# Kernel optimization log

Hardware: AMD Instinct MI355X
Metric: run time of the kernel (lower is better)

The kernel has to match this reference:

```python
import jax, jax.numpy as jnp
import numpy as np

EPS = 1e-5  # torch LayerNorm default

def setup_inputs() -> dict:
    key = jax.random.key(0)
    ks = jax.random.split(key, 4)
    S, B, D, BN = 4096, 8, 1024, 128
    x = jax.random.normal(ks[0], (S, B, D), dtype=jnp.float32)
    residual = jax.random.normal(ks[1], (B, S, D), dtype=jnp.float32)
    # xavier_uniform init for adapter projections
    lim_d = float(np.sqrt(6.0 / (D + BN)))
    W_down = jax.random.uniform(ks[2], (BN, D), minval=-lim_d, maxval=lim_d, dtype=jnp.float32)
    W_up = jax.random.uniform(ks[3], (D, BN), minval=-lim_d, maxval=lim_d, dtype=jnp.float32)
    return {
        "x": x,
        "residual": residual,
        "ln_gamma": jnp.ones((D,), jnp.float32),
        "ln_beta": jnp.zeros((D,), jnp.float32),
        "W_down": W_down,
        "b_down": jnp.zeros((BN,), jnp.float32),
        "W_up": W_up,
        "b_up": jnp.zeros((D,), jnp.float32),
    }

def reference(x, residual, ln_gamma, ln_beta, W_down, b_down, W_up, b_up):
    # ffn_fn is an opaque callable (treated as identity here); x: [S,B,D]
    x = x + jnp.swapaxes(residual, 0, 1)           # residual.transpose(0,1)
    shortcut = x
    # NaiveAdapter: LayerNorm -> down -> ReLU -> up -> residual add
    mu = jnp.mean(x, axis=-1, keepdims=True)
    var = jnp.mean(jnp.square(x - mu), axis=-1, keepdims=True)
    h = (x - mu) * jax.lax.rsqrt(var + EPS) * ln_gamma + ln_beta
    h = jax.nn.relu(jnp.einsum('sbd,kd->sbk', h, W_down) + b_down)  # [S,B,BN]
    h = jnp.einsum('sbk,dk->sbd', h, W_up) + b_up                   # [S,B,D]
    return h + shortcut
```

## Files before the change

kernel.cpp:

```cpp
#include <hip/hip_runtime.h>

#define S_DIM 4096
#define B_DIM 8
#define D_DIM 1024
#define BN_DIM 128
#define M_DIM (S_DIM * B_DIM)

typedef short s8v __attribute__((ext_vector_type(8)));
typedef float f4v __attribute__((ext_vector_type(4)));

__device__ __forceinline__ unsigned short f2bf(float f) {
  union { unsigned int i; float f; } v; v.f = f;
  unsigned int r = v.i + 0x7FFFu + ((v.i >> 16) & 1u);
  return (unsigned short)(r >> 16);
}
__device__ __forceinline__ float bf2f(unsigned short u) {
  union { unsigned int i; float f; } v; v.i = ((unsigned int)u) << 16; return v.f;
}

__global__ __launch_bounds__(256) void add_ln_kernel(
    const float* __restrict__ x,
    const float* __restrict__ res,
    const float* __restrict__ gamma,
    const float* __restrict__ beta,
    unsigned short* __restrict__ norm,
    float* __restrict__ shortcut) {
  int wave = threadIdx.x >> 6, lane = threadIdx.x & 63;
  int row = blockIdx.x * 4 + wave;
  int s = row >> 3, b = row & 7;
  const float* xr = x + (size_t)row * D_DIM;
  const float* rr = res + ((size_t)b * S_DIM + s) * D_DIM;

  float4 v[4];
  float sum = 0.f, sumsq = 0.f;
#pragma unroll
  for (int c = 0; c < 4; ++c) {
    int e = c * 256 + lane * 4;
    float4 xv = *(const float4*)&xr[e];
    float4 rv = *(const float4*)&rr[e];
    v[c].x = xv.x + rv.x; v[c].y = xv.y + rv.y;
    v[c].z = xv.z + rv.z; v[c].w = xv.w + rv.w;
    sum += v[c].x + v[c].y + v[c].z + v[c].w;
    sumsq += v[c].x * v[c].x + v[c].y * v[c].y + v[c].z * v[c].z + v[c].w * v[c].w;
  }
#pragma unroll
  for (int ofs = 32; ofs >= 1; ofs >>= 1) {
    sum   += __shfl_xor(sum, ofs, 64);
    sumsq += __shfl_xor(sumsq, ofs, 64);
  }
  float mu   = sum * (1.f / D_DIM);
  float var  = sumsq * (1.f / D_DIM) - mu * mu;
  float rstd = rsqrtf(var + 1e-5f);

  float* sr = shortcut + (size_t)row * D_DIM;
  unsigned short* nr = norm + (size_t)row * D_DIM;
#pragma unroll
  for (int c = 0; c < 4; ++c) {
    int e = c * 256 + lane * 4;
    *(float4*)&sr[e] = v[c];
    float4 gv = *(const float4*)&gamma[e];
    float4 bv = *(const float4*)&beta[e];
    ushort4 o;
    o.x = f2bf((v[c].x - mu) * rstd * gv.x + bv.x);
    o.y = f2bf((v[c].y - mu) * rstd * gv.y + bv.y);
    o.z = f2bf((v[c].z - mu) * rstd * gv.z + bv.z);
    o.w = f2bf((v[c].w - mu) * rstd * gv.w + bv.w);
    *(ushort4*)&nr[e] = o;
  }
}

#define LDT 40

__global__ __launch_bounds__(256) void gemm_down(
    const unsigned short* __restrict__ A,
    const float* __restrict__ W,
    const float* __restrict__ bias,
    unsigned short* __restrict__ H) {
  __shared__ unsigned short As[64 * LDT];
  __shared__ unsigned short Bs[128 * LDT];
  int t = threadIdx.x, wave = t >> 6, lane = t & 63;
  int tileM = blockIdx.x * 64;

  f4v acc[8];
#pragma unroll
  for (int i = 0; i < 8; ++i) acc[i] = (f4v){0.f, 0.f, 0.f, 0.f};

  int arow = t >> 2, akc = (t & 3) * 8;
  for (int kk = 0; kk < 1024; kk += 32) {
    *(s8v*)&As[arow * LDT + akc] =
        *(const s8v*)&A[(size_t)(tileM + arow) * 1024 + kk + akc];
#pragma unroll
    for (int i = 0; i < 2; ++i) {
      int idx = t + i * 256;
      int brow = idx >> 2, bkc = (idx & 3) * 8;
      const float* wp = &W[(size_t)brow * 1024 + kk + bkc];
      float4 w0 = *(const float4*)wp;
      float4 w1 = *(const float4*)(wp + 4);
      s8v bv;
      bv[0] = (short)f2bf(w0.x); bv[1] = (short)f2bf(w0.y);
      bv[2] = (short)f2bf(w0.z); bv[3] = (short)f2bf(w0.w);
      bv[4] = (short)f2bf(w1.x); bv[5] = (short)f2bf(w1.y);
      bv[6] = (short)f2bf(w1.z); bv[7] = (short)f2bf(w1.w);
      *(s8v*)&Bs[brow * LDT + bkc] = bv;
    }
    __syncthreads();
    int kq = (lane >> 4) * 8;
    s8v a = *(const s8v*)&As[(wave * 16 + (lane & 15)) * LDT + kq];
#pragma unroll
    for (int nt = 0; nt < 8; ++nt) {
      s8v b = *(const s8v*)&Bs[(nt * 16 + (lane & 15)) * LDT + kq];
      acc[nt] = __builtin_amdgcn_mfma_f32_16x16x32_bf16(a, b, acc[nt], 0, 0, 0);
    }
    __syncthreads();
  }
#pragma unroll
  for (int nt = 0; nt < 8; ++nt) {
    int n = nt * 16 + (lane & 15);
    float bs = bias[n];
#pragma unroll
    for (int r = 0; r < 4; ++r) {
      int m = wave * 16 + (lane >> 4) * 4 + r;
      float val = acc[nt][r] + bs;
      val = val > 0.f ? val : 0.f;
      H[(size_t)(tileM + m) * BN_DIM + n] = f2bf(val);
    }
  }
}

__global__ __launch_bounds__(256) void gemm_up(
    const unsigned short* __restrict__ H,
    const float* __restrict__ W,
    const float* __restrict__ bias,
    float* __restrict__ out) {
  __shared__ unsigned short As[64 * LDT];
  __shared__ unsigned short Bs[128 * LDT];
  int t = threadIdx.x, wave = t >> 6, lane = t & 63;
  int tileM = blockIdx.x * 64;
  int tileN = blockIdx.y * 128;

  f4v acc[8];
#pragma unroll
  for (int i = 0; i < 8; ++i) acc[i] = (f4v){0.f, 0.f, 0.f, 0.f};

  int arow = t >> 2, akc = (t & 3) * 8;
#pragma unroll
  for (int kk = 0; kk < 128; kk += 32) {
    *(s8v*)&As[arow * LDT + akc] =
        *(const s8v*)&H[(size_t)(tileM + arow) * BN_DIM + kk + akc];
#pragma unroll
    for (int i = 0; i < 2; ++i) {
      int idx = t + i * 256;
      int brow = idx >> 2, bkc = (idx & 3) * 8;
      const float* wp = &W[(size_t)(tileN + brow) * BN_DIM + kk + bkc];
      float4 w0 = *(const float4*)wp;
      float4 w1 = *(const float4*)(wp + 4);
      s8v bv;
      bv[0] = (short)f2bf(w0.x); bv[1] = (short)f2bf(w0.y);
      bv[2] = (short)f2bf(w0.z); bv[3] = (short)f2bf(w0.w);
      bv[4] = (short)f2bf(w1.x); bv[5] = (short)f2bf(w1.y);
      bv[6] = (short)f2bf(w1.z); bv[7] = (short)f2bf(w1.w);
      *(s8v*)&Bs[brow * LDT + bkc] = bv;
    }
    __syncthreads();
    int kq = (lane >> 4) * 8;
    s8v a = *(const s8v*)&As[(wave * 16 + (lane & 15)) * LDT + kq];
#pragma unroll
    for (int nt = 0; nt < 8; ++nt) {
      s8v b = *(const s8v*)&Bs[(nt * 16 + (lane & 15)) * LDT + kq];
      acc[nt] = __builtin_amdgcn_mfma_f32_16x16x32_bf16(a, b, acc[nt], 0, 0, 0);
    }
    __syncthreads();
  }
#pragma unroll
  for (int nt = 0; nt < 8; ++nt) {
    int n = tileN + nt * 16 + (lane & 15);
    float bs = bias[n];
#pragma unroll
    for (int r = 0; r < 4; ++r) {
      int gm = tileM + wave * 16 + (lane >> 4) * 4 + r;
      size_t oi = (size_t)gm * D_DIM + n;
      out[oi] = acc[nt][r] + bs + out[oi];
    }
  }
}

extern "C" void kernel_launch(void* const* d_in, const int* in_sizes, int n_in,
                              void* d_out, int out_size, void* d_ws, size_t ws_size,
                              hipStream_t stream) {
  const float* x      = (const float*)d_in[0];
  const float* res    = (const float*)d_in[1];
  const float* gamma  = (const float*)d_in[2];
  const float* beta   = (const float*)d_in[3];
  const float* W_down = (const float*)d_in[4];
  const float* b_down = (const float*)d_in[5];
  const float* W_up   = (const float*)d_in[6];
  const float* b_up   = (const float*)d_in[7];
  float* out = (float*)d_out;

  unsigned short* ws_norm = (unsigned short*)d_ws;
  unsigned short* ws_h1   = ws_norm + (size_t)M_DIM * D_DIM;

  add_ln_kernel<<<M_DIM / 4, 256, 0, stream>>>(x, res, gamma, beta, ws_norm, out);
  gemm_down<<<M_DIM / 64, 256, 0, stream>>>(ws_norm, W_down, b_down, ws_h1);
  gemm_up<<<dim3(M_DIM / 64, D_DIM / 128), 256, 0, stream>>>(ws_h1, W_up, b_up, out);
}
```

Before: 442.2 us.

## Fold LayerNorm affine into weights and keep bf16 residual to cut traffic

```diff
diff --git a/kernel.cpp b/kernel.cpp
--- a/kernel.cpp
+++ b/kernel.cpp
@@ -5,6 +5,8 @@
 #define D_DIM 1024
 #define BN_DIM 128
 #define M_DIM (S_DIM * B_DIM)
+#define LDT 40
+#define CLD 132
 
 typedef short s8v __attribute__((ext_vector_type(8)));
 typedef float f4v __attribute__((ext_vector_type(4)));
@@ -18,90 +20,129 @@
   union { unsigned int i; float f; } v; v.i = ((unsigned int)u) << 16; return v.f;
 }
 
+__global__ __launch_bounds__(256) void prep_kernel(
+    const float* __restrict__ Wd_f, const float* __restrict__ bd_f,
+    const float* __restrict__ Wu_f, const float* __restrict__ gamma,
+    const float* __restrict__ beta,
+    unsigned short* __restrict__ Wd, float* __restrict__ bd,
+    unsigned short* __restrict__ Wu) {
+  __shared__ float red[4];
+  int t = threadIdx.x;
+  if (blockIdx.x < 128) {
+    int n = blockIdx.x, k = t * 4;
+    float4 w = *(const float4*)&Wd_f[n * 1024 + k];
+    float4 g = *(const float4*)&gamma[k];
+    float4 bt = *(const float4*)&beta[k];
+    ushort4 o;
+    o.x = f2bf(w.x * g.x); o.y = f2bf(w.y * g.y);
+    o.z = f2bf(w.z * g.z); o.w = f2bf(w.w * g.w);
+    *(ushort4*)&Wd[n * 1024 + k] = o;
+    float bs = w.x * bt.x + w.y * bt.y + w.z * bt.z + w.w * bt.w;
+#pragma unroll
+    for (int ofs = 32; ofs >= 1; ofs >>= 1) bs += __shfl_xor(bs, ofs, 64);
+    if ((t & 63) == 0) red[t >> 6] = bs;
+    __syncthreads();
+    if (t == 0) bd[n] = bd_f[n] + red[0] + red[1] + red[2] + red[3];
+  } else {
+    int j = blockIdx.x - 128;
+#pragma unroll
+    for (int c = 0; c < 4; ++c) {
+      int idx = j * 4096 + c * 1024 + t * 4;
+      float4 w = *(const float4*)&Wu_f[idx];
+      ushort4 o;
+      o.x = f2bf(w.x); o.y = f2bf(w.y); o.z = f2bf(w.z); o.w = f2bf(w.w);
+      *(ushort4*)&Wu[idx] = o;
+    }
+    __syncthreads();
+  }
+}
+
 __global__ __launch_bounds__(256) void add_ln_kernel(
-    const float* __restrict__ x,
-    const float* __restrict__ res,
-    const float* __restrict__ gamma,
-    const float* __restrict__ beta,
-    unsigned short* __restrict__ norm,
-    float* __restrict__ shortcut) {
+    const float* __restrict__ x, const float* __restrict__ res,
+    unsigned short* __restrict__ y, float2* __restrict__ stats) {
   int wave = threadIdx.x >> 6, lane = threadIdx.x & 63;
-  int row = blockIdx.x * 4 + wave;
-  int s = row >> 3, b = row & 7;
-  const float* xr = x + (size_t)row * D_DIM;
-  const float* rr = res + ((size_t)b * S_DIM + s) * D_DIM;
-
-  float4 v[4];
-  float sum = 0.f, sumsq = 0.f;
-#pragma unroll
-  for (int c = 0; c < 4; ++c) {
-    int e = c * 256 + lane * 4;
-    float4 xv = *(const float4*)&xr[e];
-    float4 rv = *(const float4*)&rr[e];
-    v[c].x = xv.x + rv.x; v[c].y = xv.y + rv.y;
-    v[c].z = xv.z + rv.z; v[c].w = xv.w + rv.w;
-    sum += v[c].x + v[c].y + v[c].z + v[c].w;
-    sumsq += v[c].x * v[c].x + v[c].y * v[c].y + v[c].z * v[c].z + v[c].w * v[c].w;
-  }
+  int row0 = blockIdx.x * 8 + wave * 2;
+
+  float4 xa[2][4], ra[2][4];
+#pragma unroll
+  for (int p = 0; p < 2; ++p) {
+    int row = row0 + p;
+    const float* xr = x + (size_t)row * D_DIM;
+    const float* rr = res + ((size_t)(row & 7) * S_DIM + (row >> 3)) * D_DIM;
+#pragma unroll
+    for (int c = 0; c < 4; ++c) {
+      int e = c * 256 + lane * 4;
+      xa[p][c] = *(const float4*)&xr[e];
+      ra[p][c] = *(const float4*)&rr[e];
+    }
+  }
+  float sum[2] = {0.f, 0.f}, sq[2] = {0.f, 0.f};
+#pragma unroll
+  for (int p = 0; p < 2; ++p)
+#pragma unroll
+    for (int c = 0; c < 4; ++c) {
+      xa[p][c].x += ra[p][c].x; xa[p][c].y += ra[p][c].y;
+      xa[p][c].z += ra[p][c].z; xa[p][c].w += ra[p][c].w;
+      sum[p] += xa[p][c].x + xa[p][c].y + xa[p][c].z + xa[p][c].w;
+      sq[p] += xa[p][c].x * xa[p][c].x + xa[p][c].y * xa[p][c].y +
+               xa[p][c].z * xa[p][c].z + xa[p][c].w * xa[p][c].w;
+    }
 #pragma unroll
   for (int ofs = 32; ofs >= 1; ofs >>= 1) {
-    sum   += __shfl_xor(sum, ofs, 64);
-    sumsq += __shfl_xor(sumsq, ofs, 64);
-  }
-  float mu   = sum * (1.f / D_DIM);
-  float var  = sumsq * (1.f / D_DIM) - mu * mu;
-  float rstd = rsqrtf(var + 1e-5f);
-
-  float* sr = shortcut + (size_t)row * D_DIM;
-  unsigned short* nr = norm + (size_t)row * D_DIM;
-#pragma unroll
-  for (int c = 0; c < 4; ++c) {
-    int e = c * 256 + lane * 4;
-    *(float4*)&sr[e] = v[c];
-    float4 gv = *(const float4*)&gamma[e];
-    float4 bv = *(const float4*)&beta[e];
-    ushort4 o;
-    o.x = f2bf((v[c].x - mu) * rstd * gv.x + bv.x);
-    o.y = f2bf((v[c].y - mu) * rstd * gv.y + bv.y);
-    o.z = f2bf((v[c].z - mu) * rstd * gv.z + bv.z);
-    o.w = f2bf((v[c].w - mu) * rstd * gv.w + bv.w);
-    *(ushort4*)&nr[e] = o;
-  }
-}
-
-#define LDT 40
+    sum[0] += __shfl_xor(sum[0], ofs, 64);
+    sq[0]  += __shfl_xor(sq[0], ofs, 64);
+    sum[1] += __shfl_xor(sum[1], ofs, 64);
+    sq[1]  += __shfl_xor(sq[1], ofs, 64);
+  }
+#pragma unroll
+  for (int p = 0; p < 2; ++p) {
+    int row = row0 + p;
+    float mu = sum[p] * (1.f / D_DIM);
+    float var = sq[p] * (1.f / D_DIM) - mu * mu;
+    float rstd = rsqrtf(var + 1e-5f);
+    if (lane == 0) stats[row] = make_float2(mu, rstd);
+    unsigned short* yr = y + (size_t)row * D_DIM;
+#pragma unroll
+    for (int c = 0; c < 4; ++c) {
+      int e = c * 256 + lane * 4;
+      ushort4 o;
+      o.x = f2bf(xa[p][c].x); o.y = f2bf(xa[p][c].y);
+      o.z = f2bf(xa[p][c].z); o.w = f2bf(xa[p][c].w);
+      *(ushort4*)&yr[e] = o;
+    }
+  }
+}
 
 __global__ __launch_bounds__(256) void gemm_down(
-    const unsigned short* __restrict__ A,
-    const float* __restrict__ W,
-    const float* __restrict__ bias,
+    const unsigned short* __restrict__ Y,
+    const unsigned short* __restrict__ Wd,
+    const float* __restrict__ bd,
+    const float2* __restrict__ stats,
     unsigned short* __restrict__ H) {
   __shared__ unsigned short As[64 * LDT];
   __shared__ unsigned short Bs[128 * LDT];
   int t = threadIdx.x, wave = t >> 6, lane = t & 63;
   int tileM = blockIdx.x * 64;
+  int arow = t >> 2, akc = (t & 3) * 8;
+  float2 st = stats[tileM + arow];
+  float rstd = st.y, nmu = -st.x * st.y;
 
   f4v acc[8];
 #pragma unroll
   for (int i = 0; i < 8; ++i) acc[i] = (f4v){0.f, 0.f, 0.f, 0.f};
 
-  int arow = t >> 2, akc = (t & 3) * 8;
   for (int kk = 0; kk < 1024; kk += 32) {
-    *(s8v*)&As[arow * LDT + akc] =
-        *(const s8v*)&A[(size_t)(tileM + arow) * 1024 + kk + akc];
+    s8v yv = *(const s8v*)&Y[(size_t)(tileM + arow) * 1024 + kk + akc];
+    s8v av;
+#pragma unroll
+    for (int j = 0; j < 8; ++j)
+      av[j] = (short)f2bf(bf2f((unsigned short)yv[j]) * rstd + nmu);
+    *(s8v*)&As[arow * LDT + akc] = av;
 #pragma unroll
     for (int i = 0; i < 2; ++i) {
       int idx = t + i * 256;
       int brow = idx >> 2, bkc = (idx & 3) * 8;
-      const float* wp = &W[(size_t)brow * 1024 + kk + bkc];
-      float4 w0 = *(const float4*)wp;
-      float4 w1 = *(const float4*)(wp + 4);
-      s8v bv;
-      bv[0] = (short)f2bf(w0.x); bv[1] = (short)f2bf(w0.y);
-      bv[2] = (short)f2bf(w0.z); bv[3] = (short)f2bf(w0.w);
-      bv[4] = (short)f2bf(w1.x); bv[5] = (short)f2bf(w1.y);
-      bv[6] = (short)f2bf(w1.z); bv[7] = (short)f2bf(w1.w);
-      *(s8v*)&Bs[brow * LDT + bkc] = bv;
+      *(s8v*)&Bs[brow * LDT + bkc] = *(const s8v*)&Wd[(size_t)brow * 1024 + kk + bkc];
     }
     __syncthreads();
     int kq = (lane >> 4) * 8;
@@ -116,7 +157,7 @@
 #pragma unroll
   for (int nt = 0; nt < 8; ++nt) {
     int n = nt * 16 + (lane & 15);
-    float bs = bias[n];
+    float bs = bd[n];
 #pragma unroll
     for (int r = 0; r < 4; ++r) {
       int m = wave * 16 + (lane >> 4) * 4 + r;
@@ -129,11 +170,13 @@
 
 __global__ __launch_bounds__(256) void gemm_up(
     const unsigned short* __restrict__ H,
-    const float* __restrict__ W,
+    const unsigned short* __restrict__ Wu,
     const float* __restrict__ bias,
+    const unsigned short* __restrict__ Y,
     float* __restrict__ out) {
   __shared__ unsigned short As[64 * LDT];
   __shared__ unsigned short Bs[128 * LDT];
+  __shared__ float Cs[64 * CLD];
   int t = threadIdx.x, wave = t >> 6, lane = t & 63;
   int tileM = blockIdx.x * 64;
   int tileN = blockIdx.y * 128;
@@ -151,15 +194,8 @@
     for (int i = 0; i < 2; ++i) {
       int idx = t + i * 256;
       int brow = idx >> 2, bkc = (idx & 3) * 8;
-      const float* wp = &W[(size_t)(tileN + brow) * BN_DIM + kk + bkc];
-      float4 w0 = *(const float4*)wp;
-      float4 w1 = *(const float4*)(wp + 4);
-      s8v bv;
-      bv[0] = (short)f2bf(w0.x); bv[1] = (short)f2bf(w0.y);
-      bv[2] = (short)f2bf(w0.z); bv[3] = (short)f2bf(w0.w);
-      bv[4] = (short)f2bf(w1.x); bv[5] = (short)f2bf(w1.y);
-      bv[6] = (short)f2bf(w1.z); bv[7] = (short)f2bf(w1.w);
-      *(s8v*)&Bs[brow * LDT + bkc] = bv;
+      *(s8v*)&Bs[brow * LDT + bkc] =
+          *(const s8v*)&Wu[(size_t)(tileN + brow) * BN_DIM + kk + bkc];
     }
     __syncthreads();
     int kq = (lane >> 4) * 8;
@@ -173,14 +209,33 @@
   }
 #pragma unroll
   for (int nt = 0; nt < 8; ++nt) {
-    int n = tileN + nt * 16 + (lane & 15);
-    float bs = bias[n];
+    int nl = nt * 16 + (lane & 15);
+    float bs = bias[tileN + nl];
 #pragma unroll
     for (int r = 0; r < 4; ++r) {
-      int gm = tileM + wave * 16 + (lane >> 4) * 4 + r;
-      size_t oi = (size_t)gm * D_DIM + n;
-      out[oi] = acc[nt][r] + bs + out[oi];
-    }
+      int m = wave * 16 + (lane >> 4) * 4 + r;
+      Cs[m * CLD + nl] = acc[nt][r] + bs;
+    }
+  }
+  __syncthreads();
+#pragma unroll
+  for (int pass = 0; pass < 4; ++pass) {
+    int m = pass * 16 + (t >> 4);
+    int col = (t & 15) * 8;
+    size_t gbase = (size_t)(tileM + m) * D_DIM + tileN + col;
+    s8v yv = *(const s8v*)&Y[gbase];
+    const float* cs = &Cs[m * CLD + col];
+    float4 o0, o1;
+    o0.x = cs[0] + bf2f((unsigned short)yv[0]);
+    o0.y = cs[1] + bf2f((unsigned short)yv[1]);
+    o0.z = cs[2] + bf2f((unsigned short)yv[2]);
+    o0.w = cs[3] + bf2f((unsigned short)yv[3]);
+    o1.x = cs[4] + bf2f((unsigned short)yv[4]);
+    o1.y = cs[5] + bf2f((unsigned short)yv[5]);
+    o1.z = cs[6] + bf2f((unsigned short)yv[6]);
+    o1.w = cs[7] + bf2f((unsigned short)yv[7]);
+    *(float4*)&out[gbase] = o0;
+    *(float4*)&out[gbase + 4] = o1;
   }
 }
 
@@ -197,10 +252,17 @@
   const float* b_up   = (const float*)d_in[7];
   float* out = (float*)d_out;
 
-  unsigned short* ws_norm = (unsigned short*)d_ws;
-  unsigned short* ws_h1   = ws_norm + (size_t)M_DIM * D_DIM;
-
-  add_ln_kernel<<<M_DIM / 4, 256, 0, stream>>>(x, res, gamma, beta, ws_norm, out);
-  gemm_down<<<M_DIM / 64, 256, 0, stream>>>(ws_norm, W_down, b_down, ws_h1);
-  gemm_up<<<dim3(M_DIM / 64, D_DIM / 128), 256, 0, stream>>>(ws_h1, W_up, b_up, out);
-}
+  unsigned short* ws_y  = (unsigned short*)d_ws;
+  unsigned short* ws_h1 = ws_y + (size_t)M_DIM * D_DIM;
+  float2* ws_stats      = (float2*)(ws_h1 + (size_t)M_DIM * BN_DIM);
+  unsigned short* ws_wd = (unsigned short*)(ws_stats + M_DIM);
+  float* ws_bd          = (float*)(ws_wd + 128 * 1024);
+  unsigned short* ws_wu = (unsigned short*)(ws_bd + 128);
+
+  prep_kernel<<<160, 256, 0, stream>>>(W_down, b_down, W_up, gamma, beta,
+                                       ws_wd, ws_bd, ws_wu);
+  add_ln_kernel<<<M_DIM / 8, 256, 0, stream>>>(x, res, ws_y, ws_stats);
+  gemm_down<<<M_DIM / 64, 256, 0, stream>>>(ws_y, ws_wd, ws_bd, ws_stats, ws_h1);
+  gemm_up<<<dim3(M_DIM / 64, D_DIM / 128), 256, 0, stream>>>(ws_h1, ws_wu, b_up,
+                                                             ws_y, out);
+}
```

Result: faster. 416.0 us (-5.9%).
